# Optimization experiments

Hardware: AMD Instinct MI355X
Metric: run time of the kernel (lower is better)

## Reference

```python
import jax, jax.numpy as jnp
import numpy as np


def dct_matrix(T):
    # Orthonormal DCT-II matrix: y = D @ x  (torch_dct.dct(..., norm='ortho'))
    n = jnp.arange(T, dtype=jnp.float32)
    k = jnp.arange(T, dtype=jnp.float32)[:, None]
    D = jnp.cos(jnp.pi * (n + 0.5) * k / T) * np.sqrt(2.0 / T)
    D = D.at[0].mul(1.0 / np.sqrt(2.0))
    return D.astype(jnp.float32)


def setup_inputs() -> dict:
    key = jax.random.key(0)
    k1, k2, k3 = jax.random.split(key, 3)
    B, C, T, H, W = 8, 64, 16, 64, 64
    text_dim = 768
    r = jax.random.normal(k1, (B, C, T, H, W), dtype=jnp.float32)
    E_txt = jax.random.normal(k2, (B, text_dim), dtype=jnp.float32)
    Wf = jax.random.normal(k3, (C * T, text_dim), dtype=jnp.float32) * 0.02
    bf = jnp.zeros((C * T,), dtype=jnp.float32)
    return {"r": r, "E_txt": E_txt, "Wf": Wf, "bf": bf}


def reference(r, E_txt, Wf, bf):
    B, C, T, H, W = r.shape
    D = dct_matrix(T)  # (T, T), orthonormal so IDCT = D.T
    # DCT-II along the T axis (avoids materializing permuted copies)
    r_freq = jnp.einsum('bcthw,kt->bckhw', r, D)
    # sigmoid-gated per-(B,C,T) frequency modulation
    w = jax.nn.sigmoid((E_txt @ Wf.T + bf).reshape(B, C, T, 1, 1))
    mod = r_freq * w
    # inverse DCT (DCT-III ortho) along the frequency axis back to T
    r_out = jnp.einsum('bckhw,kt->bcthw', mod, D)
    return r_out
```

## Files before the change

### kernel.cpp

```cpp
#include <hip/hip_runtime.h>
#include <math.h>


#define HW4 1024

__global__ __launch_bounds__(256) void gate_kernel(
    const float* __restrict__ E,
    const float* __restrict__ Wf,
    const float* __restrict__ bf,
    float* __restrict__ wout)
{
    const int wave = threadIdx.x >> 6;
    const int lane = threadIdx.x & 63;
    const int ct   = blockIdx.x * 4 + wave;

    const float4* W4 = (const float4*)(Wf) + ct * 192;
    const float4* E4 = (const float4*)E;

    float acc[8];
#pragma unroll
    for (int b = 0; b < 8; ++b) acc[b] = 0.f;

#pragma unroll
    for (int j = 0; j < 3; ++j) {
        float4 a = W4[j * 64 + lane];
#pragma unroll
        for (int b = 0; b < 8; ++b) {
            float4 e = E4[b * 192 + j * 64 + lane];
            acc[b] = fmaf(a.x, e.x, acc[b]);
            acc[b] = fmaf(a.y, e.y, acc[b]);
            acc[b] = fmaf(a.z, e.z, acc[b]);
            acc[b] = fmaf(a.w, e.w, acc[b]);
        }
    }
#pragma unroll
    for (int off = 32; off >= 1; off >>= 1) {
#pragma unroll
        for (int b = 0; b < 8; ++b)
            acc[b] += __shfl_xor(acc[b], off, 64);
    }
    const float bias = bf[ct];
#pragma unroll
    for (int b = 0; b < 8; ++b) {
        if (lane == b) {
            float s = acc[b] + bias;
            wout[b * 1024 + ct] = 1.0f / (1.0f + expf(-s));
        }
    }
}

__global__ __launch_bounds__(256) void buildM_kernel(
    const float* __restrict__ wbuf,
    float* __restrict__ Mout)
{
    __shared__ float Dl[16][16];
    __shared__ float wv[16];
    const int tid = threadIdx.x;
    const int bc  = blockIdx.x;
    {
        int k = tid >> 4, n = tid & 15;
        float v = (k == 0) ? 0.25f
                           : cospif((n + 0.5f) * (float)k * (1.0f / 16.0f)) * 0.35355339059327373f;
        Dl[k][n] = v;
        if (tid < 16) wv[tid] = wbuf[bc * 16 + tid];
    }
    __syncthreads();
    int i = tid >> 4, j = tid & 15;
    float s = 0.f;
#pragma unroll
    for (int k = 0; k < 16; ++k)
        s = fmaf(Dl[k][i] * wv[k], Dl[k][j], s);
    Mout[bc * 256 + tid] = s;
}

__global__ __launch_bounds__(64) void mod_kernel(
    const float* __restrict__ r,
    const float* __restrict__ M,
    float* __restrict__ out)
{
    __shared__ float4 Ms4[64];
    const int lane  = threadIdx.x;
    const int bc    = blockIdx.x >> 4;
    const int chunk = blockIdx.x & 15;

    Ms4[lane] = ((const float4*)(M + bc * 256))[lane];
    __syncthreads();
    const float* Ms = (const float*)Ms4;

    const size_t base = (size_t)bc * (16 * 4096);
    const float4* rp = (const float4*)(r + base);
    float4*       op = (float4*)(out + base);
    const int col = chunk * 64 + lane;

    float4 x[16];
#pragma unroll
    for (int k = 0; k < 16; ++k)
        x[k] = rp[k * HW4 + col];

    float4 y[16];
#pragma unroll
    for (int t = 0; t < 16; ++t)
        y[t] = make_float4(0.f, 0.f, 0.f, 0.f);

#pragma unroll
    for (int k = 0; k < 16; ++k) {
        float4 xk = x[k];
#pragma unroll
        for (int t = 0; t < 16; ++t) {
            float m = Ms[t * 16 + k];
            y[t].x = fmaf(m, xk.x, y[t].x);
            y[t].y = fmaf(m, xk.y, y[t].y);
            y[t].z = fmaf(m, xk.z, y[t].z);
            y[t].w = fmaf(m, xk.w, y[t].w);
        }
    }

#pragma unroll
    for (int t = 0; t < 16; ++t)
        op[t * HW4 + col] = y[t];
}

extern "C" void kernel_launch(void* const* d_in, const int* in_sizes, int n_in,
                              void* d_out, int out_size, void* d_ws, size_t ws_size,
                              hipStream_t stream) {
    const float* r  = (const float*)d_in[0];
    const float* E  = (const float*)d_in[1];
    const float* Wf = (const float*)d_in[2];
    const float* bf = (const float*)d_in[3];
    float* out = (float*)d_out;
    float* w   = (float*)d_ws;
    float* M   = (float*)d_ws + 8192;

    gate_kernel  <<<256, 256, 0, stream>>>(E, Wf, bf, w);
    buildM_kernel<<<512, 256, 0, stream>>>(w, M);
    mod_kernel   <<<8192, 64, 0, stream>>>(r, M, out);
}
```

Before: 243.6 us.

## Fuse M construction into modulation kernel with streamed nontemporal loads

Removes the separate buildM kernel: each 256-thread block of the modulation kernel now builds its 16x16 gated DCT matrix in shared memory, storing it transposed so it can be read as float4 rows. The initial loads of r are issued before the matrix build so memory latency overlaps that work. Loads stream through a rolling 4-deep register buffer rather than holding all 16 rows, and both loads and stores use nontemporal hints. This cuts one launch and an intermediate global round trip, and lowers register pressure. The cost is that every block recomputes M, so each (b,c) matrix is now built four times instead of once.

```diff
diff --git a/kernel.cpp b/kernel.cpp
--- a/kernel.cpp
+++ b/kernel.cpp
@@ -3,6 +3,8 @@
 
 
 #define HW4 1024
+
+typedef float f4 __attribute__((ext_vector_type(4)));
 
 __global__ __launch_bounds__(256) void gate_kernel(
     const float* __restrict__ E,
@@ -49,14 +51,31 @@
     }
 }
 
-__global__ __launch_bounds__(256) void buildM_kernel(
+__global__ __launch_bounds__(256, 4) void mod_kernel(
+    const float* __restrict__ r,
     const float* __restrict__ wbuf,
-    float* __restrict__ Mout)
+    float* __restrict__ out)
 {
     __shared__ float Dl[16][16];
     __shared__ float wv[16];
-    const int tid = threadIdx.x;
-    const int bc  = blockIdx.x;
+    __shared__ __align__(16) float Ms[256];
+
+    const int tid   = threadIdx.x;
+    const int wave  = tid >> 6;
+    const int lane  = tid & 63;
+    const int bc    = blockIdx.x >> 2;
+    const int chunk = (blockIdx.x & 3) * 4 + wave;
+
+    const size_t base = (size_t)bc * (16 * 4096);
+    const f4* rp = (const f4*)(r + base);
+    f4*       op = (f4*)(out + base);
+    const int col = chunk * 64 + lane;
+
+    f4 xb[4];
+#pragma unroll
+    for (int k = 0; k < 4; ++k)
+        xb[k] = __builtin_nontemporal_load(&rp[k * HW4 + col]);
+
     {
         int k = tid >> 4, n = tid & 15;
         float v = (k == 0) ? 0.25f
@@ -65,59 +84,52 @@
         if (tid < 16) wv[tid] = wbuf[bc * 16 + tid];
     }
     __syncthreads();
-    int i = tid >> 4, j = tid & 15;
-    float s = 0.f;
+    {
+        int i = tid >> 4, j = tid & 15;
+        float s = 0.f;
 #pragma unroll
-    for (int k = 0; k < 16; ++k)
-        s = fmaf(Dl[k][i] * wv[k], Dl[k][j], s);
-    Mout[bc * 256 + tid] = s;
-}
+        for (int k = 0; k < 16; ++k)
+            s = fmaf(Dl[k][i] * wv[k], Dl[k][j], s);
+        Ms[j * 16 + i] = s;
+    }
+    __syncthreads();
 
-__global__ __launch_bounds__(64) void mod_kernel(
-    const float* __restrict__ r,
-    const float* __restrict__ M,
-    float* __restrict__ out)
-{
-    __shared__ float4 Ms4[64];
-    const int lane  = threadIdx.x;
-    const int bc    = blockIdx.x >> 4;
-    const int chunk = blockIdx.x & 15;
-
-    Ms4[lane] = ((const float4*)(M + bc * 256))[lane];
-    __syncthreads();
-    const float* Ms = (const float*)Ms4;
-
-    const size_t base = (size_t)bc * (16 * 4096);
-    const float4* rp = (const float4*)(r + base);
-    float4*       op = (float4*)(out + base);
-    const int col = chunk * 64 + lane;
-
-    float4 x[16];
-#pragma unroll
-    for (int k = 0; k < 16; ++k)
-        x[k] = rp[k * HW4 + col];
-
-    float4 y[16];
+    f4 y[16];
 #pragma unroll
     for (int t = 0; t < 16; ++t)
-        y[t] = make_float4(0.f, 0.f, 0.f, 0.f);
+        y[t] = (f4){0.f, 0.f, 0.f, 0.f};
 
 #pragma unroll
     for (int k = 0; k < 16; ++k) {
-        float4 xk = x[k];
+        f4 xk = xb[k & 3];
+        if (k + 4 < 16)
+            xb[k & 3] = __builtin_nontemporal_load(&rp[(k + 4) * HW4 + col]);
+        const f4* Mk = (const f4*)(Ms + k * 16);
 #pragma unroll
-        for (int t = 0; t < 16; ++t) {
-            float m = Ms[t * 16 + k];
-            y[t].x = fmaf(m, xk.x, y[t].x);
-            y[t].y = fmaf(m, xk.y, y[t].y);
-            y[t].z = fmaf(m, xk.z, y[t].z);
-            y[t].w = fmaf(m, xk.w, y[t].w);
+        for (int t4 = 0; t4 < 4; ++t4) {
+            f4 m = Mk[t4];
+            y[4 * t4 + 0].x = fmaf(m.x, xk.x, y[4 * t4 + 0].x);
+            y[4 * t4 + 0].y = fmaf(m.x, xk.y, y[4 * t4 + 0].y);
+            y[4 * t4 + 0].z = fmaf(m.x, xk.z, y[4 * t4 + 0].z);
+            y[4 * t4 + 0].w = fmaf(m.x, xk.w, y[4 * t4 + 0].w);
+            y[4 * t4 + 1].x = fmaf(m.y, xk.x, y[4 * t4 + 1].x);
+            y[4 * t4 + 1].y = fmaf(m.y, xk.y, y[4 * t4 + 1].y);
+            y[4 * t4 + 1].z = fmaf(m.y, xk.z, y[4 * t4 + 1].z);
+            y[4 * t4 + 1].w = fmaf(m.y, xk.w, y[4 * t4 + 1].w);
+            y[4 * t4 + 2].x = fmaf(m.z, xk.x, y[4 * t4 + 2].x);
+            y[4 * t4 + 2].y = fmaf(m.z, xk.y, y[4 * t4 + 2].y);
+            y[4 * t4 + 2].z = fmaf(m.z, xk.z, y[4 * t4 + 2].z);
+            y[4 * t4 + 2].w = fmaf(m.z, xk.w, y[4 * t4 + 2].w);
+            y[4 * t4 + 3].x = fmaf(m.w, xk.x, y[4 * t4 + 3].x);
+            y[4 * t4 + 3].y = fmaf(m.w, xk.y, y[4 * t4 + 3].y);
+            y[4 * t4 + 3].z = fmaf(m.w, xk.z, y[4 * t4 + 3].z);
+            y[4 * t4 + 3].w = fmaf(m.w, xk.w, y[4 * t4 + 3].w);
         }
     }
 
 #pragma unroll
     for (int t = 0; t < 16; ++t)
-        op[t * HW4 + col] = y[t];
+        __builtin_nontemporal_store(y[t], &op[t * HW4 + col]);
 }
 
 extern "C" void kernel_launch(void* const* d_in, const int* in_sizes, int n_in,
@@ -129,9 +141,7 @@
     const float* bf = (const float*)d_in[3];
     float* out = (float*)d_out;
     float* w   = (float*)d_ws;
-    float* M   = (float*)d_ws + 8192;
 
-    gate_kernel  <<<256, 256, 0, stream>>>(E, Wf, bf, w);
-    buildM_kernel<<<512, 256, 0, stream>>>(w, M);
-    mod_kernel   <<<8192, 64, 0, stream>>>(r, M, out);
+    gate_kernel<<<256, 256, 0, stream>>>(E, Wf, bf, w);
+    mod_kernel <<<2048, 256, 0, stream>>>(r, w, out);
 }
```

Result: no change. 240.3 us (-1.4%).
